# Kernel optimization log

Hardware: AMD Instinct MI355X
Metric: run time of the kernel (lower is better)

Reference implementation:

```python
import jax, jax.numpy as jnp
import numpy as np

EPS = 1e-06
CHUNK = 128  # chunkwise-recurrent block size for causal linear attention


def _feature_map(x):
    # elu(x) + 1, strictly positive kernel feature map
    return jax.nn.elu(x) + 1.0


def setup_inputs() -> dict:
    key = jax.random.key(0)
    kq, kk, kv = jax.random.split(key, 3)
    shape = (4, 4096, 16, 64)  # [N, L, H, D]
    return {
        "queries": jax.random.normal(kq, shape, dtype=jnp.float32),
        "keys": jax.random.normal(kk, shape, dtype=jnp.float32),
        "values": jax.random.normal(kv, shape, dtype=jnp.float32),
    }


def reference(queries, keys, values):
    # Causal linear attention: out_l = phi(q_l) . (sum_{s<=l} phi(k_s) v_s^T) / (phi(q_l) . sum_{s<=l} phi(k_s))
    q = _feature_map(queries)  # [N, L, H, D]
    k = _feature_map(keys)
    n, L, h, d = q.shape
    m = values.shape[-1]

    # Normalizer: z_l = q_l . cumsum(k)_l  (+ eps)
    z = jnp.einsum('nlhd,nlhd->nlh', q, jnp.cumsum(k, axis=1)) + EPS  # [N, L, H]

    # Chunkwise causal k (x) v accumulation
    g = L // CHUNK
    qc = q.reshape(n, g, CHUNK, h, d)
    kc = k.reshape(n, g, CHUNK, h, d)
    vc = values.reshape(n, g, CHUNK, h, m)

    # Per-chunk KV state and exclusive prefix over chunks
    kv = jnp.einsum('ngchd,ngchm->nghdm', kc, vc)  # [N, G, H, D, M]
    kv_cum = jnp.cumsum(kv, axis=1)
    kv_prev = jnp.concatenate([jnp.zeros_like(kv_cum[:, :1]), kv_cum[:, :-1]], axis=1)

    # Inter-chunk contribution (history before this chunk)
    inter = jnp.einsum('ngchd,nghdm->ngchm', qc, kv_prev)  # [N, G, C, H, M]

    # Intra-chunk causal contribution via lower-triangular masked scores
    scores = jnp.einsum('ngchd,ngkhd->nghck', qc, kc)  # [N, G, H, C, C]
    tri = jnp.tril(jnp.ones((CHUNK, CHUNK), dtype=bool))
    scores = jnp.where(tri[None, None, None], scores, 0.0)
    intra = jnp.einsum('nghck,ngkhm->ngchm', scores, vc)  # [N, G, C, H, M]

    num = (inter + intra).reshape(n, L, h, m)
    return num / z[..., None]
```

## Files before the change

### kernel.cpp

```cpp
#include <hip/hip_runtime.h>
#include <math.h>

static constexpr int Nn = 4, Ll = 4096, Hh = 16, Dd = 64, Mm = 64, Cc = 128, Gg = 32;
static constexpr int ROWS = Hh * Dd;
#define EPS_ 1e-6f

typedef __bf16 bf16x8 __attribute__((ext_vector_type(8)));
typedef unsigned short us8 __attribute__((ext_vector_type(8)));
typedef float f32x4 __attribute__((ext_vector_type(4)));

__device__ __forceinline__ float phi(float x) {
    return x > 0.0f ? x + 1.0f : __expf(x);
}

__device__ __forceinline__ unsigned short f2bf(float x) {
    unsigned u = __float_as_uint(x);
    return (unsigned short)((u + 0x7fffu + ((u >> 16) & 1u)) >> 16);
}
__device__ __forceinline__ float bf2f(unsigned short h) {
    return __uint_as_float(((unsigned)h) << 16);
}

#define MFMA16(A, B, C)                                                      \
    __builtin_amdgcn_mfma_f32_16x16x32_bf16(__builtin_bit_cast(bf16x8, (A)), \
                                            __builtin_bit_cast(bf16x8, (B)), \
                                            (C), 0, 0, 0)

__device__ __forceinline__ int KIDX(int j, int d) {
    return j * 64 + ((((d >> 3) ^ j) & 7) << 3) + (d & 7);
}
__device__ __forceinline__ int VTIDX(int m, int j) {
    return m * 128 + ((((j >> 3) ^ (m & 15) ^ (m >> 4)) & 15) << 3) + (j & 7);
}

__device__ __forceinline__ void load8(const float* p, float* xs) {
    float4 a = *(const float4*)p, b = *(const float4*)(p + 4);
    xs[0] = a.x; xs[1] = a.y; xs[2] = a.z; xs[3] = a.w;
    xs[4] = b.x; xs[5] = b.y; xs[6] = b.z; xs[7] = b.w;
}

__device__ __forceinline__ void unpack8(const unsigned* p, us8& hi, us8& lo) {
    const uint4 a = *(const uint4*)p;
    const uint4 b = *(const uint4*)(p + 4);
    union { unsigned u[4]; us8 v; } H, L;
    H.u[0] = __builtin_amdgcn_perm(a.y, a.x, 0x05040100u);
    L.u[0] = __builtin_amdgcn_perm(a.y, a.x, 0x07060302u);
    H.u[1] = __builtin_amdgcn_perm(a.w, a.z, 0x05040100u);
    L.u[1] = __builtin_amdgcn_perm(a.w, a.z, 0x07060302u);
    H.u[2] = __builtin_amdgcn_perm(b.y, b.x, 0x05040100u);
    L.u[2] = __builtin_amdgcn_perm(b.y, b.x, 0x07060302u);
    H.u[3] = __builtin_amdgcn_perm(b.w, b.z, 0x05040100u);
    L.u[3] = __builtin_amdgcn_perm(b.w, b.z, 0x07060302u);
    hi = H.v; lo = L.v;
}

__global__ __launch_bounds__(256, 2) void kv_state_kernel(
    const float* __restrict__ keys, const float* __restrict__ values,
    float* __restrict__ kvbuf, float* __restrict__ ksumbuf)
{
    __shared__ alignas(16) unsigned short KthS[64 * 128];
    __shared__ alignas(16) unsigned short KtlS[64 * 128];
    __shared__ alignas(16) unsigned short VthS[64 * 128];
    __shared__ alignas(16) unsigned short VtlS[64 * 128];

    const int b = blockIdx.x;
    const int h = b % Hh;
    const int g = (b / Hh) % Gg;
    const int n = b / (Hh * Gg);
    const int tid = threadIdx.x;

    const size_t inbase = ((size_t)(n * Ll + g * Cc) * Hh + h) * Dd;

    for (int i = tid; i < 1024; i += 256) {
        const int jp = i >> 4, d4 = (i & 15) * 4;
        const int c0 = jp * 2;
        const float4 ka = *(const float4*)(keys   + inbase + (size_t)c0 * ROWS + d4);
        const float4 kb = *(const float4*)(keys   + inbase + (size_t)(c0 + 1) * ROWS + d4);
        const float4 va = *(const float4*)(values + inbase + (size_t)c0 * ROWS + d4);
        const float4 vb = *(const float4*)(values + inbase + (size_t)(c0 + 1) * ROWS + d4);
        const float kaa[4] = {ka.x, ka.y, ka.z, ka.w};
        const float kbb[4] = {kb.x, kb.y, kb.z, kb.w};
        const float vaa[4] = {va.x, va.y, va.z, va.w};
        const float vbb[4] = {vb.x, vb.y, vb.z, vb.w};
        #pragma unroll
        for (int e = 0; e < 4; ++e) {
            const int idx = VTIDX(d4 + e, c0);
            const float pa = phi(kaa[e]), pb = phi(kbb[e]);
            const unsigned ha = f2bf(pa), hb = f2bf(pb);
            *(unsigned*)(KthS + idx) = ha | (hb << 16);
            const unsigned la = f2bf(pa - bf2f((unsigned short)ha));
            const unsigned lb = f2bf(pb - bf2f((unsigned short)hb));
            *(unsigned*)(KtlS + idx) = la | (lb << 16);
            const unsigned hva = f2bf(vaa[e]), hvb = f2bf(vbb[e]);
            *(unsigned*)(VthS + idx) = hva | (hvb << 16);
            const unsigned lva = f2bf(vaa[e] - bf2f((unsigned short)hva));
            const unsigned lvb = f2bf(vbb[e] - bf2f((unsigned short)hvb));
            *(unsigned*)(VtlS + idx) = lva | (lvb << 16);
        }
    }
    __syncthreads();

    const int w = tid >> 6, l = tid & 63;
    const int lr = l & 15, lg = l >> 4;

    us8 ah[4], al[4];
    #pragma unroll
    for (int cs = 0; cs < 4; ++cs) {
        ah[cs] = *(const us8*)(VthS + VTIDX(w * 16 + lr, cs * 32 + lg * 8));
        al[cs] = *(const us8*)(VtlS + VTIDX(w * 16 + lr, cs * 32 + lg * 8));
    }

    float* kvout = kvbuf + ((size_t)((n * Gg + g) * Hh + h)) * (Dd * Mm);
    __builtin_amdgcn_s_setprio(1);
    #pragma unroll
    for (int dt = 0; dt < 4; ++dt) {
        f32x4 acc = {0.f, 0.f, 0.f, 0.f};
        #pragma unroll
        for (int cs = 0; cs < 4; ++cs) {
            us8 bh = *(const us8*)(KthS + VTIDX(dt * 16 + lr, cs * 32 + lg * 8));
            us8 bl = *(const us8*)(KtlS + VTIDX(dt * 16 + lr, cs * 32 + lg * 8));
            acc = MFMA16(ah[cs], bh, acc);
            acc = MFMA16(ah[cs], bl, acc);
            acc = MFMA16(al[cs], bh, acc);
        }
        #pragma unroll
        for (int r = 0; r < 4; ++r)
            kvout[(size_t)(w * 16 + lg * 4 + r) * 64 + dt * 16 + lr] = acc[r];
    }
    __builtin_amdgcn_s_setprio(0);

    if (tid < 64) {
        float s = 0.f;
        #pragma unroll
        for (int gb = 0; gb < 16; ++gb) {
            us8 hh = *(const us8*)(KthS + VTIDX(tid, gb * 8));
            us8 ll = *(const us8*)(KtlS + VTIDX(tid, gb * 8));
            #pragma unroll
            for (int e = 0; e < 8; ++e) s += bf2f(hh[e]) + bf2f(ll[e]);
        }
        ksumbuf[((size_t)((n * Gg + g) * Hh + h)) * 64 + tid] = s;
    }
}

__global__ __launch_bounds__(256) void prefix_kernel(
    float* __restrict__ kvbuf, float* __restrict__ ksumbuf)
{
    const int t = blockIdx.x * 256 + threadIdx.x;
    const int NKV = Nn * Hh * Dd * Mm;
    if (t < NKV) {
        const int nh = t >> 12, dm = t & 4095;
        const int n = nh >> 4, h = nh & 15;
        unsigned* kvp = (unsigned*)kvbuf;
        float run = 0.f;
        for (int g = 0; g < Gg; ++g) {
            const size_t idx = ((size_t)((n * Gg + g) * Hh + h)) * 4096 + dm;
            const float v = kvbuf[idx];
            const unsigned hb = f2bf(run);
            const unsigned lb = f2bf(run - bf2f((unsigned short)hb));
            kvp[idx] = hb | (lb << 16);
            run += v;
        }
    } else {
        const int t2 = t - NKV;
        if (t2 < Nn * Hh * Dd) {
            const int nh = t2 >> 6, d = t2 & 63;
            const int n = nh >> 4, h = nh & 15;
            float run = 0.f;
            for (int g = 0; g < Gg; ++g) {
                const size_t idx = ((size_t)((n * Gg + g) * Hh + h)) * 64 + d;
                const float v = ksumbuf[idx];
                ksumbuf[idx] = run;
                run += v;
            }
        }
    }
}

__global__ __launch_bounds__(256, 2) void out_kernel(
    const float* __restrict__ queries,
    const float* __restrict__ keys,
    const float* __restrict__ values,
    const float* __restrict__ kvbuf,
    const float* __restrict__ ksumbuf,
    float* __restrict__ out)
{
    __shared__ alignas(16) unsigned short KhS[128 * 64];
    __shared__ alignas(16) unsigned short KlS[128 * 64];
    __shared__ alignas(16) unsigned short VthS[64 * 128];
    __shared__ alignas(16) unsigned short VtlS[64 * 128];
    __shared__ alignas(16) unsigned short SshS[4 * 512];
    __shared__ alignas(16) unsigned short SslS[4 * 512];
    __shared__ float kpreS[64];

    const int b = blockIdx.x;
    const int h = b & 15, g = (b >> 4) & 31, n = b >> 9;
    const int tid = threadIdx.x;

    const size_t chunkbase = ((size_t)(n * Ll + g * Cc) * Hh + h) * Dd;
    const size_t stateoff  = (size_t)((n * Gg + g) * Hh + h);

    if (tid < 16)
        *(float4*)(kpreS + tid * 4) =
            *(const float4*)(ksumbuf + stateoff * 64 + tid * 4);

    for (int t = tid; t < 1024; t += 256) {
        const int j = t >> 3, gb = t & 7;
        float xs[8];
        load8(keys + chunkbase + (size_t)j * ROWS + gb * 8, xs);
        us8 hh, ll;
        #pragma unroll
        for (int e = 0; e < 8; ++e) {
            const float p = phi(xs[e]);
            const unsigned short hb = f2bf(p);
            hh[e] = hb; ll[e] = f2bf(p - bf2f(hb));
        }
        const int base = KIDX(j, gb * 8);
        *(us8*)(KhS + base) = hh;
        *(us8*)(KlS + base) = ll;
    }
    for (int t = tid; t < 1024; t += 256) {
        const int jp = t >> 4, m4 = (t & 15) * 4;
        const int j0 = jp * 2;
        const float4 va = *(const float4*)(values + chunkbase + (size_t)j0 * ROWS + m4);
        const float4 vb = *(const float4*)(values + chunkbase + (size_t)(j0 + 1) * ROWS + m4);
        const float vaa[4] = {va.x, va.y, va.z, va.w};
        const float vbb[4] = {vb.x, vb.y, vb.z, vb.w};
        #pragma unroll
        for (int e = 0; e < 4; ++e) {
            const int idx = VTIDX(m4 + e, j0);
            const unsigned hva = f2bf(vaa[e]), hvb = f2bf(vbb[e]);
            *(unsigned*)(VthS + idx) = hva | (hvb << 16);
            const unsigned lva = f2bf(vaa[e] - bf2f((unsigned short)hva));
            const unsigned lvb = f2bf(vbb[e] - bf2f((unsigned short)hvb));
            *(unsigned*)(VtlS + idx) = lva | (lvb << 16);
        }
    }
    __syncthreads();

    const int w = tid >> 6, l = tid & 63;
    const int lr = l & 15, lg = l >> 4;
    const unsigned* kvpk = (const unsigned*)kvbuf + stateoff * (size_t)4096;

    for (int tt = 0; tt < 2; ++tt) {
        const int T = tt ? (7 - w) : w;

        us8 qh[2], ql[2];
        float u = 0.f;
        #pragma unroll
        for (int ks = 0; ks < 2; ++ks) {
            float xs[8];
            load8(queries + chunkbase + (size_t)(T * 16 + lr) * ROWS + ks * 32 + lg * 8, xs);
            us8 hh, ll;
            #pragma unroll
            for (int e = 0; e < 8; ++e) {
                const float p = phi(xs[e]);
                u += p * kpreS[ks * 32 + lg * 8 + e];
                const unsigned short hb = f2bf(p);
                hh[e] = hb; ll[e] = f2bf(p - bf2f(hb));
            }
            qh[ks] = hh; ql[ks] = ll;
        }
        u += __shfl_xor(u, 16, 64);
        u += __shfl_xor(u, 32, 64);

        f32x4 accO[4];
        #pragma unroll
        for (int mt = 0; mt < 4; ++mt) {
            const unsigned* p = kvpk + (size_t)(mt * 16 + lr) * 64 + lg * 8;
            us8 bh0, bl0, bh1, bl1;
            unpack8(p, bh0, bl0);
            unpack8(p + 32, bh1, bl1);
            f32x4 acc = {0.f, 0.f, 0.f, 0.f};
            acc = MFMA16(qh[0], bh0, acc);
            acc = MFMA16(qh[0], bl0, acc);
            acc = MFMA16(ql[0], bh0, acc);
            acc = MFMA16(qh[1], bh1, acc);
            acc = MFMA16(qh[1], bl1, acc);
            acc = MFMA16(ql[1], bh1, acc);
            accO[mt] = acc;
        }

        f32x4 zp = {0.f, 0.f, 0.f, 0.f};
        const int nJb = (T + 2) >> 1;
        for (int Jb = 0; Jb < nJb; ++Jb) {
            const int Jlo = 2 * Jb, Jhi = 2 * Jb + 1;
            const bool hasHi = (Jhi <= T);

            f32x4 slo = {0.f, 0.f, 0.f, 0.f};
            f32x4 shi = {0.f, 0.f, 0.f, 0.f};
            __builtin_amdgcn_s_setprio(1);
            #pragma unroll
            for (int ks = 0; ks < 2; ++ks) {
                us8 bh = *(const us8*)(KhS + KIDX(Jlo * 16 + lr, ks * 32 + lg * 8));
                us8 bl = *(const us8*)(KlS + KIDX(Jlo * 16 + lr, ks * 32 + lg * 8));
                slo = MFMA16(qh[ks], bh, slo);
                slo = MFMA16(qh[ks], bl, slo);
                slo = MFMA16(ql[ks], bh, slo);
            }
            if (hasHi) {
                #pragma unroll
                for (int ks = 0; ks < 2; ++ks) {
                    us8 bh = *(const us8*)(KhS + KIDX(Jhi * 16 + lr, ks * 32 + lg * 8));
                    us8 bl = *(const us8*)(KlS + KIDX(Jhi * 16 + lr, ks * 32 + lg * 8));
                    shi = MFMA16(qh[ks], bh, shi);
                    shi = MFMA16(qh[ks], bl, shi);
                    shi = MFMA16(ql[ks], bh, shi);
                }
            }
            __builtin_amdgcn_s_setprio(0);
            if (Jlo == T) {
                #pragma unroll
                for (int r = 0; r < 4; ++r)
                    if (lr > lg * 4 + r) slo[r] = 0.f;
            }
            if (hasHi && Jhi == T) {
                #pragma unroll
                for (int r = 0; r < 4; ++r)
                    if (lr > lg * 4 + r) shi[r] = 0.f;
            }
            zp += slo;
            zp += shi;

            unsigned short* sh = SshS + w * 512;
            unsigned short* sl = SslS + w * 512;
            #pragma unroll
            for (int r = 0; r < 4; ++r) {
                const int row = lg * 4 + r;
                const unsigned short h0 = f2bf(slo[r]);
                sh[row * 32 + lr]      = h0;
                sl[row * 32 + lr]      = f2bf(slo[r] - bf2f(h0));
                const unsigned short h1 = f2bf(shi[r]);
                sh[row * 32 + 16 + lr] = h1;
                sl[row * 32 + 16 + lr] = f2bf(shi[r] - bf2f(h1));
            }
            asm volatile("s_waitcnt lgkmcnt(0)" ::: "memory");
            __builtin_amdgcn_sched_barrier(0);

            us8 ah = *(const us8*)(sh + lr * 32 + lg * 8);
            us8 al = *(const us8*)(sl + lr * 32 + lg * 8);
            __builtin_amdgcn_s_setprio(1);
            #pragma unroll
            for (int mt = 0; mt < 4; ++mt) {
                us8 vh = *(const us8*)(VthS + VTIDX(mt * 16 + lr, Jb * 32 + lg * 8));
                us8 vl = *(const us8*)(VtlS + VTIDX(mt * 16 + lr, Jb * 32 + lg * 8));
                accO[mt] = MFMA16(ah, vh, accO[mt]);
                accO[mt] = MFMA16(ah, vl, accO[mt]);
                accO[mt] = MFMA16(al, vh, accO[mt]);
            }
            __builtin_amdgcn_s_setprio(0);
        }

        #pragma unroll
        for (int r = 0; r < 4; ++r) {
            float s = zp[r];
            s += __shfl_xor(s, 1, 64);
            s += __shfl_xor(s, 2, 64);
            s += __shfl_xor(s, 4, 64);
            s += __shfl_xor(s, 8, 64);
            zp[r] = s;
        }

        const size_t ob = ((size_t)(n * Ll + g * Cc + T * 16) * Hh + h) * Mm;
        #pragma unroll
        for (int r = 0; r < 4; ++r) {
            const int row = lg * 4 + r;
            const float ur = __shfl(u, row, 64);
            const float iz = 1.0f / (EPS_ + ur + zp[r]);
            #pragma unroll
            for (int mt = 0; mt < 4; ++mt)
                out[ob + (size_t)row * ROWS + mt * 16 + lr] = accO[mt][r] * iz;
        }
    }
}

extern "C" void kernel_launch(void* const* d_in, const int* in_sizes, int n_in,
                              void* d_out, int out_size, void* d_ws, size_t ws_size,
                              hipStream_t stream) {
    const float* q = (const float*)d_in[0];
    const float* k = (const float*)d_in[1];
    const float* v = (const float*)d_in[2];
    float* out = (float*)d_out;

    float* kvbuf   = (float*)d_ws;
    float* ksumbuf = kvbuf + (size_t)Nn * Gg * Hh * Dd * Mm;

    kv_state_kernel<<<Nn * Gg * Hh, 256, 0, stream>>>(k, v, kvbuf, ksumbuf);

    const int nseries = Nn * Hh * Dd * Mm + Nn * Hh * Dd;
    prefix_kernel<<<nseries / 256, 256, 0, stream>>>(kvbuf, ksumbuf);

    out_kernel<<<Nn * Gg * Hh, 256, 0, stream>>>(q, k, v, kvbuf, ksumbuf, out);
}
```

Measured before the change: 285.8 us.

## Fuse per-chunk KV state and prefix scan into one sequential scan kernel

Replaces the per-chunk kv_state kernel and the separate prefix kernel with a single kernel in which each block owns one (n,h,m-tile). It walks all 32 chunks sequentially, accumulating the KV state in MFMA registers, writes the exclusive prefix as packed bf16 hi/lo, and prefetches the next chunk's keys and values into registers. This removes a launch and the float KV round-trip through global memory. The trade-off is a grid of only 256 blocks, each doing serial chunk iterations, with keys staged redundantly by the four m-tile blocks. The output kernel also issues its query loads early, before the shared-memory staging, to overlap their latency.

```diff
diff --git a/kernel.cpp b/kernel.cpp
--- a/kernel.cpp
+++ b/kernel.cpp
@@ -54,124 +54,129 @@
     hi = H.v; lo = L.v;
 }
 
-__global__ __launch_bounds__(256, 2) void kv_state_kernel(
+struct KVPf {
+    float4 ka0, kb0, ka1, kb1, ka2, kb2, ka3, kb3;
+    float4 va, vb;
+};
+
+#define KV_LD(A, B, C, D) (*(const float4*)((A) + (B) + (size_t)(C) * ROWS + (D)))
+
+#define KV_PF_LOAD(G, P) do {                                                  \
+    const size_t gb_ = ((size_t)(n * Ll + (G) * Cc) * Hh + h) * Dd;            \
+    { const int u_ = tid;       const int d4_ = (u_ & 15) * 4, c0_ = (u_ >> 4) * 2; \
+      P.ka0 = KV_LD(keys, gb_, c0_, d4_); P.kb0 = KV_LD(keys, gb_, c0_ + 1, d4_); } \
+    { const int u_ = tid + 256; const int d4_ = (u_ & 15) * 4, c0_ = (u_ >> 4) * 2; \
+      P.ka1 = KV_LD(keys, gb_, c0_, d4_); P.kb1 = KV_LD(keys, gb_, c0_ + 1, d4_); } \
+    { const int u_ = tid + 512; const int d4_ = (u_ & 15) * 4, c0_ = (u_ >> 4) * 2; \
+      P.ka2 = KV_LD(keys, gb_, c0_, d4_); P.kb2 = KV_LD(keys, gb_, c0_ + 1, d4_); } \
+    { const int u_ = tid + 768; const int d4_ = (u_ & 15) * 4, c0_ = (u_ >> 4) * 2; \
+      P.ka3 = KV_LD(keys, gb_, c0_, d4_); P.kb3 = KV_LD(keys, gb_, c0_ + 1, d4_); } \
+    { const int m4_ = (tid & 3) * 4 + mt * 16, c0_ = (tid >> 2) * 2;           \
+      P.va = KV_LD(values, gb_, c0_, m4_); P.vb = KV_LD(values, gb_, c0_ + 1, m4_); } \
+} while (0)
+
+#define STAGE_K_UNIT(IT, KA, KB) do {                                          \
+    const int unit_ = tid + (IT) * 256;                                        \
+    const int d4_ = (unit_ & 15) * 4, c0_ = (unit_ >> 4) * 2;                  \
+    const float kaa_[4] = {KA.x, KA.y, KA.z, KA.w};                            \
+    const float kbb_[4] = {KB.x, KB.y, KB.z, KB.w};                            \
+    _Pragma("unroll")                                                          \
+    for (int e = 0; e < 4; ++e) {                                              \
+        const int idx = VTIDX(d4_ + e, c0_);                                   \
+        const float pa = phi(kaa_[e]), pb = phi(kbb_[e]);                      \
+        const unsigned ha = f2bf(pa), hb2 = f2bf(pb);                          \
+        *(unsigned*)(KthS + idx) = ha | (hb2 << 16);                           \
+        const unsigned la = f2bf(pa - bf2f((unsigned short)ha));               \
+        const unsigned lb2 = f2bf(pb - bf2f((unsigned short)hb2));             \
+        *(unsigned*)(KtlS + idx) = la | (lb2 << 16);                           \
+    }                                                                          \
+} while (0)
+
+__global__ __launch_bounds__(256) void kv_scan_kernel(
     const float* __restrict__ keys, const float* __restrict__ values,
-    float* __restrict__ kvbuf, float* __restrict__ ksumbuf)
+    unsigned* __restrict__ kvbuf, float* __restrict__ ksumbuf)
 {
     __shared__ alignas(16) unsigned short KthS[64 * 128];
     __shared__ alignas(16) unsigned short KtlS[64 * 128];
-    __shared__ alignas(16) unsigned short VthS[64 * 128];
-    __shared__ alignas(16) unsigned short VtlS[64 * 128];
-
-    const int b = blockIdx.x;
-    const int h = b % Hh;
-    const int g = (b / Hh) % Gg;
-    const int n = b / (Hh * Gg);
+    __shared__ alignas(16) unsigned short VmhS[16 * 128];
+    __shared__ alignas(16) unsigned short VmlS[16 * 128];
+    __shared__ float ksP[4 * 64];
+
+    const int bid = blockIdx.x;
+    const int mt = bid >> 6;
+    const int grp = bid & 63;
+    const int n = grp >> 4, h = grp & 15;
     const int tid = threadIdx.x;
-
-    const size_t inbase = ((size_t)(n * Ll + g * Cc) * Hh + h) * Dd;
-
-    for (int i = tid; i < 1024; i += 256) {
-        const int jp = i >> 4, d4 = (i & 15) * 4;
-        const int c0 = jp * 2;
-        const float4 ka = *(const float4*)(keys   + inbase + (size_t)c0 * ROWS + d4);
-        const float4 kb = *(const float4*)(keys   + inbase + (size_t)(c0 + 1) * ROWS + d4);
-        const float4 va = *(const float4*)(values + inbase + (size_t)c0 * ROWS + d4);
-        const float4 vb = *(const float4*)(values + inbase + (size_t)(c0 + 1) * ROWS + d4);
-        const float kaa[4] = {ka.x, ka.y, ka.z, ka.w};
-        const float kbb[4] = {kb.x, kb.y, kb.z, kb.w};
-        const float vaa[4] = {va.x, va.y, va.z, va.w};
-        const float vbb[4] = {vb.x, vb.y, vb.z, vb.w};
-        #pragma unroll
-        for (int e = 0; e < 4; ++e) {
-            const int idx = VTIDX(d4 + e, c0);
-            const float pa = phi(kaa[e]), pb = phi(kbb[e]);
-            const unsigned ha = f2bf(pa), hb = f2bf(pb);
-            *(unsigned*)(KthS + idx) = ha | (hb << 16);
-            const unsigned la = f2bf(pa - bf2f((unsigned short)ha));
-            const unsigned lb = f2bf(pb - bf2f((unsigned short)hb));
-            *(unsigned*)(KtlS + idx) = la | (lb << 16);
-            const unsigned hva = f2bf(vaa[e]), hvb = f2bf(vbb[e]);
-            *(unsigned*)(VthS + idx) = hva | (hvb << 16);
-            const unsigned lva = f2bf(vaa[e] - bf2f((unsigned short)hva));
-            const unsigned lvb = f2bf(vbb[e] - bf2f((unsigned short)hvb));
-            *(unsigned*)(VtlS + idx) = lva | (lvb << 16);
-        }
-    }
-    __syncthreads();
-
     const int w = tid >> 6, l = tid & 63;
     const int lr = l & 15, lg = l >> 4;
 
-    us8 ah[4], al[4];
-    #pragma unroll
-    for (int cs = 0; cs < 4; ++cs) {
-        ah[cs] = *(const us8*)(VthS + VTIDX(w * 16 + lr, cs * 32 + lg * 8));
-        al[cs] = *(const us8*)(VtlS + VTIDX(w * 16 + lr, cs * 32 + lg * 8));
-    }
-
-    float* kvout = kvbuf + ((size_t)((n * Gg + g) * Hh + h)) * (Dd * Mm);
-    __builtin_amdgcn_s_setprio(1);
-    #pragma unroll
-    for (int dt = 0; dt < 4; ++dt) {
-        f32x4 acc = {0.f, 0.f, 0.f, 0.f};
+    KVPf pf;
+    KV_PF_LOAD(0, pf);
+
+    f32x4 acc = {0.f, 0.f, 0.f, 0.f};
+    float runk = 0.f;
+
+    for (int g = 0; g < Gg; ++g) {
+        STAGE_K_UNIT(0, pf.ka0, pf.kb0);
+        STAGE_K_UNIT(1, pf.ka1, pf.kb1);
+        STAGE_K_UNIT(2, pf.ka2, pf.kb2);
+        STAGE_K_UNIT(3, pf.ka3, pf.kb3);
+        {
+            const int m4 = (tid & 3) * 4, c0 = (tid >> 2) * 2;
+            const float vaa[4] = {pf.va.x, pf.va.y, pf.va.z, pf.va.w};
+            const float vbb[4] = {pf.vb.x, pf.vb.y, pf.vb.z, pf.vb.w};
+            #pragma unroll
+            for (int e = 0; e < 4; ++e) {
+                const int idx = VTIDX(m4 + e, c0);
+                const unsigned ha = f2bf(vaa[e]), hb2 = f2bf(vbb[e]);
+                *(unsigned*)(VmhS + idx) = ha | (hb2 << 16);
+                const unsigned la = f2bf(vaa[e] - bf2f((unsigned short)ha));
+                const unsigned lb2 = f2bf(vbb[e] - bf2f((unsigned short)hb2));
+                *(unsigned*)(VmlS + idx) = la | (lb2 << 16);
+            }
+        }
+        __syncthreads();
+
+        if (g + 1 < Gg) KV_PF_LOAD(g + 1, pf);
+
+        {
+            unsigned* kvp = kvbuf + ((size_t)((n * Gg + g) * Hh + h)) * 4096;
+            #pragma unroll
+            for (int r = 0; r < 4; ++r) {
+                const unsigned hb = f2bf(acc[r]);
+                const unsigned lb = f2bf(acc[r] - bf2f((unsigned short)hb));
+                kvp[(mt * 16 + lg * 4 + r) * 64 + w * 16 + lr] = hb | (lb << 16);
+            }
+        }
+
         #pragma unroll
         for (int cs = 0; cs < 4; ++cs) {
-            us8 bh = *(const us8*)(KthS + VTIDX(dt * 16 + lr, cs * 32 + lg * 8));
-            us8 bl = *(const us8*)(KtlS + VTIDX(dt * 16 + lr, cs * 32 + lg * 8));
-            acc = MFMA16(ah[cs], bh, acc);
-            acc = MFMA16(ah[cs], bl, acc);
-            acc = MFMA16(al[cs], bh, acc);
-        }
-        #pragma unroll
-        for (int r = 0; r < 4; ++r)
-            kvout[(size_t)(w * 16 + lg * 4 + r) * 64 + dt * 16 + lr] = acc[r];
-    }
-    __builtin_amdgcn_s_setprio(0);
-
-    if (tid < 64) {
-        float s = 0.f;
-        #pragma unroll
-        for (int gb = 0; gb < 16; ++gb) {
-            us8 hh = *(const us8*)(KthS + VTIDX(tid, gb * 8));
-            us8 ll = *(const us8*)(KtlS + VTIDX(tid, gb * 8));
-            #pragma unroll
-            for (int e = 0; e < 8; ++e) s += bf2f(hh[e]) + bf2f(ll[e]);
-        }
-        ksumbuf[((size_t)((n * Gg + g) * Hh + h)) * 64 + tid] = s;
-    }
-}
-
-__global__ __launch_bounds__(256) void prefix_kernel(
-    float* __restrict__ kvbuf, float* __restrict__ ksumbuf)
-{
-    const int t = blockIdx.x * 256 + threadIdx.x;
-    const int NKV = Nn * Hh * Dd * Mm;
-    if (t < NKV) {
-        const int nh = t >> 12, dm = t & 4095;
-        const int n = nh >> 4, h = nh & 15;
-        unsigned* kvp = (unsigned*)kvbuf;
-        float run = 0.f;
-        for (int g = 0; g < Gg; ++g) {
-            const size_t idx = ((size_t)((n * Gg + g) * Hh + h)) * 4096 + dm;
-            const float v = kvbuf[idx];
-            const unsigned hb = f2bf(run);
-            const unsigned lb = f2bf(run - bf2f((unsigned short)hb));
-            kvp[idx] = hb | (lb << 16);
-            run += v;
-        }
-    } else {
-        const int t2 = t - NKV;
-        if (t2 < Nn * Hh * Dd) {
-            const int nh = t2 >> 6, d = t2 & 63;
-            const int n = nh >> 4, h = nh & 15;
-            float run = 0.f;
-            for (int g = 0; g < Gg; ++g) {
-                const size_t idx = ((size_t)((n * Gg + g) * Hh + h)) * 64 + d;
-                const float v = ksumbuf[idx];
-                ksumbuf[idx] = run;
-                run += v;
-            }
+            us8 a_h = *(const us8*)(VmhS + VTIDX(lr, cs * 32 + lg * 8));
+            us8 a_l = *(const us8*)(VmlS + VTIDX(lr, cs * 32 + lg * 8));
+            us8 b_h = *(const us8*)(KthS + VTIDX(w * 16 + lr, cs * 32 + lg * 8));
+            us8 b_l = *(const us8*)(KtlS + VTIDX(w * 16 + lr, cs * 32 + lg * 8));
+            acc = MFMA16(a_h, b_h, acc);
+            acc = MFMA16(a_h, b_l, acc);
+            acc = MFMA16(a_l, b_h, acc);
+        }
+
+        if (mt == 0) {
+            const int d = tid & 63, q = tid >> 6;
+            float s = 0.f;
+            #pragma unroll
+            for (int sq = 0; sq < 4; ++sq) {
+                us8 hh = *(const us8*)(KthS + VTIDX(d, q * 32 + sq * 8));
+                us8 ll = *(const us8*)(KtlS + VTIDX(d, q * 32 + sq * 8));
+                #pragma unroll
+                for (int e = 0; e < 8; ++e) s += bf2f(hh[e]) + bf2f(ll[e]);
+            }
+            ksP[q * 64 + d] = s;
+        }
+        __syncthreads();
+        if (mt == 0 && tid < 64) {
+            const float sg = ksP[tid] + ksP[64 + tid] + ksP[128 + tid] + ksP[192 + tid];
+            ksumbuf[((size_t)((n * Gg + g) * Hh + h)) * 64 + tid] = runk;
+            runk += sg;
         }
     }
 }
@@ -195,9 +200,24 @@
     const int b = blockIdx.x;
     const int h = b & 15, g = (b >> 4) & 31, n = b >> 9;
     const int tid = threadIdx.x;
+    const int w = tid >> 6, l = tid & 63;
+    const int lr = l & 15, lg = l >> 4;
 
     const size_t chunkbase = ((size_t)(n * Ll + g * Cc) * Hh + h) * Dd;
     const size_t stateoff  = (size_t)((n * Gg + g) * Hh + h);
+
+    float4 qv[2][2][2];
+    #pragma unroll
+    for (int tt = 0; tt < 2; ++tt) {
+        const int T = tt ? (7 - w) : w;
+        #pragma unroll
+        for (int ks = 0; ks < 2; ++ks) {
+            const float* qp = queries + chunkbase +
+                              (size_t)(T * 16 + lr) * ROWS + ks * 32 + lg * 8;
+            qv[tt][ks][0] = *(const float4*)qp;
+            qv[tt][ks][1] = *(const float4*)(qp + 4);
+        }
+    }
 
     if (tid < 16)
         *(float4*)(kpreS + tid * 4) =
@@ -237,10 +257,9 @@
     }
     __syncthreads();
 
-    const int w = tid >> 6, l = tid & 63;
-    const int lr = l & 15, lg = l >> 4;
     const unsigned* kvpk = (const unsigned*)kvbuf + stateoff * (size_t)4096;
 
+    #pragma unroll
     for (int tt = 0; tt < 2; ++tt) {
         const int T = tt ? (7 - w) : w;
 
@@ -248,8 +267,8 @@
         float u = 0.f;
         #pragma unroll
         for (int ks = 0; ks < 2; ++ks) {
-            float xs[8];
-            load8(queries + chunkbase + (size_t)(T * 16 + lr) * ROWS + ks * 32 + lg * 8, xs);
+            const float4 xa = qv[tt][ks][0], xb = qv[tt][ks][1];
+            const float xs[8] = {xa.x, xa.y, xa.z, xa.w, xb.x, xb.y, xb.z, xb.w};
             us8 hh, ll;
             #pragma unroll
             for (int e = 0; e < 8; ++e) {
@@ -381,13 +400,11 @@
     const float* v = (const float*)d_in[2];
     float* out = (float*)d_out;
 
-    float* kvbuf   = (float*)d_ws;
-    float* ksumbuf = kvbuf + (size_t)Nn * Gg * Hh * Dd * Mm;
-
-    kv_state_kernel<<<Nn * Gg * Hh, 256, 0, stream>>>(k, v, kvbuf, ksumbuf);
-
-    const int nseries = Nn * Hh * Dd * Mm + Nn * Hh * Dd;
-    prefix_kernel<<<nseries / 256, 256, 0, stream>>>(kvbuf, ksumbuf);
-
-    out_kernel<<<Nn * Gg * Hh, 256, 0, stream>>>(q, k, v, kvbuf, ksumbuf, out);
-}
+    unsigned* kvbuf = (unsigned*)d_ws;
+    float* ksumbuf  = (float*)d_ws + (size_t)Nn * Gg * Hh * Dd * Mm;
+
+    kv_scan_kernel<<<Nn * Hh * 4, 256, 0, stream>>>(k, v, kvbuf, ksumbuf);
+
+    out_kernel<<<Nn * Gg * Hh, 256, 0, stream>>>(q, k, v, (const float*)kvbuf,
+                                                 ksumbuf, out);
+}
```

Result: slower. 310.0 us (+8.5%).
